# Optimization experiments

Measured on AMD Instinct MI355X. Metric: run time of the kernel, lower is better.

## Reference

```python
import jax, jax.numpy as jnp
import numpy as np

B, N_QUBITS, N_LAYERS = 128, 14, 4


def _rx(theta):
    c = jnp.cos(theta / 2).astype(jnp.complex64)
    s = (-1j) * jnp.sin(theta / 2).astype(jnp.complex64)
    return jnp.stack([jnp.stack([c, s], -1), jnp.stack([s, c], -1)], -2)


def _ry(theta):
    c = jnp.cos(theta / 2)
    s = jnp.sin(theta / 2)
    return jnp.stack([jnp.stack([c, -s], -1), jnp.stack([s, c], -1)], -2).astype(jnp.complex64)


def _rz(theta):
    p = jnp.exp((-0.5j) * theta.astype(jnp.complex64))
    q = jnp.exp((0.5j) * theta.astype(jnp.complex64))
    z = jnp.zeros_like(p)
    return jnp.stack([jnp.stack([p, z], -1), jnp.stack([z, q], -1)], -2)


def _apply_1q(state, U, wire):
    # state: (B, 2, 2, ..., 2); U: (2,2) shared or (B,2,2) per-sample
    s = jnp.moveaxis(state, wire + 1, 1)
    if U.ndim == 2:
        s = jnp.einsum('ij,bj...->bi...', U, s)
    else:
        s = jnp.einsum('bij,bj...->bi...', U, s)
    return jnp.moveaxis(s, 1, wire + 1)


def _cnot(state, c, t):
    s = jnp.moveaxis(state, (c + 1, t + 1), (1, 2))  # (B, 2c, 2t, rest)
    s = jnp.concatenate([s[:, :1], s[:, 1:, ::-1]], axis=1)  # flip target where control=1
    return jnp.moveaxis(s, (1, 2), (c + 1, t + 1))


def _layer(state, rx_l, ry_l, rz_l, ent_l, n):
    for i in range(n):
        state = _apply_1q(state, _rx(rx_l[i]), i)
        state = _apply_1q(state, _ry(ry_l[i]), i)
        state = _apply_1q(state, _rz(rz_l[i]), i)
    for i in range(n - 1):
        state = _cnot(state, i, i + 1)
        state = _apply_1q(state, _rz(ent_l[i]), i + 1)
    return state


def _circuit(x, rx_p, ry_p, rz_p, ent_p):
    b, n = x.shape
    n_layers = rx_p.shape[0]
    scaled = jnp.tanh(x) * np.pi  # angle encoding, matches torch.tanh(x)*pi
    state = jnp.zeros((b,) + (2,) * n, jnp.complex64)
    state = state.at[(slice(None),) + (0,) * n].set(1.0)  # |0...0> per sample
    for i in range(n):  # per-sample RY encoding
        state = _apply_1q(state, _ry(scaled[:, i]), i)
    for l in range(n_layers):
        state = _layer(state, rx_p[l], ry_p[l], rz_p[l], ent_p[l], n)
    probs = state.real ** 2 + state.imag ** 2  # (B, 2, ..., 2) real
    outs = []
    for i in range(n):  # <Z_i> = P(bit_i=0) - P(bit_i=1)
        p = jnp.moveaxis(probs, i + 1, 1).reshape(b, 2, -1).sum(-1)
        outs.append(p[:, 0] - p[:, 1])
    return jnp.stack(outs, -1)  # (B, n_qubits)


def setup_inputs() -> dict:
    key = jax.random.key(0)
    k1, k2, k3, k4, k5 = jax.random.split(key, 5)
    return {
        'x': jax.random.normal(k1, (B, N_QUBITS), jnp.float32),
        'params_rx': jax.random.normal(k2, (N_LAYERS, N_QUBITS), jnp.float32),
        'params_ry': jax.random.normal(k3, (N_LAYERS, N_QUBITS), jnp.float32),
        'params_rz': jax.random.normal(k4, (N_LAYERS, N_QUBITS), jnp.float32),
        'params_entangle': jax.random.normal(k5, (N_LAYERS, N_QUBITS - 1), jnp.float32),
    }


def reference(x, params_rx, params_ry, params_rz, params_entangle):
    return _circuit(x, params_rx, params_ry, params_rz, params_entangle)
```

## Files before the change

kernel.cpp:

```cpp
#include <hip/hip_runtime.h>
#include <math.h>

#define NQ 14
#define NL 4
#define NS (1 << NQ)
#define NT 1024
#define APT (NS / NT)

struct c32 { float x, y; };
__device__ __forceinline__ c32 cmul(c32 a, c32 b) { return {a.x*b.x - a.y*b.y, a.x*b.y + a.y*b.x}; }
__device__ __forceinline__ c32 cadd(c32 a, c32 b) { return {a.x + b.x, a.y + b.y}; }

template<int L> __device__ __forceinline__ int permP(int y) {
    if constexpr (L == 0) return y;
    else if constexpr (L == 1) return y ^ (y >> 1);
    else if constexpr (L == 2) return y ^ (y >> 2);
    else if constexpr (L == 3) { int t = y ^ (y >> 1); return t ^ (t >> 2); }
    else return y ^ (y >> 4);
}

__device__ __forceinline__ void gate8(c32* v, const float* U, const int s) {
    c32 u00={U[0],U[1]}, u01={U[2],U[3]}, u10={U[4],U[5]}, u11={U[6],U[7]};
    #pragma unroll
    for (int k = 0; k < 8; ++k) {
        if (k & s) continue;
        c32 A = v[k], B = v[k | s];
        v[k]     = cadd(cmul(u00, A), cmul(u01, B));
        v[k | s] = cadd(cmul(u10, A), cmul(u11, B));
    }
}

__device__ __forceinline__ void gate8sw(c32* v, const float* U, const int s, const int sw) {
    c32 u00 = sw ? c32{U[6],U[7]} : c32{U[0],U[1]};
    c32 u01 = sw ? c32{U[4],U[5]} : c32{U[2],U[3]};
    c32 u10 = sw ? c32{U[2],U[3]} : c32{U[4],U[5]};
    c32 u11 = sw ? c32{U[0],U[1]} : c32{U[6],U[7]};
    #pragma unroll
    for (int k = 0; k < 8; ++k) {
        if (k & s) continue;
        c32 A = v[k], B = v[k | s];
        v[k]     = cadd(cmul(u00, A), cmul(u01, B));
        v[k | s] = cadd(cmul(u10, A), cmul(u11, B));
    }
}

template<int L, int PB, bool FUSE>
__device__ __forceinline__ void sweep3(float2* st,
                                       const float* U2, const float* U1, const float* U0,
                                       const float* phlo, const float* phhi, int tid) {
    #pragma unroll 1
    for (int m = 0; m < 2; ++m) {
        const int t  = tid + m*NT;
        const int ib = ((t >> PB) << (PB+3)) | (t & ((1 << PB) - 1));
        c32 v[8]; int ad[8];
        #pragma unroll
        for (int k = 0; k < 8; ++k) {
            int y = ib + (k << PB);
            int a = permP<L>(y);
            ad[k] = a;
            float2 f = st[a];
            c32 vv = {f.x, f.y};
            if constexpr (FUSE) {
                float ang = phlo[y & 127] + phhi[(y >> 7) & 63];
                float sn, cs;
                __sincosf(ang, &sn, &cs);
                vv = { cs*vv.x - sn*vv.y, cs*vv.y + sn*vv.x };
            }
            v[k] = vv;
        }
        gate8(v, U2, 4);
        gate8(v, U1, 2);
        gate8(v, U0, 1);
        #pragma unroll
        for (int k = 0; k < 8; ++k) st[ad[k]] = make_float2(v[k].x, v[k].y);
    }
}

template<int L>
__device__ __forceinline__ void sweep2_43(float2* st, const float* U4, const float* U3, int tid) {
    #pragma unroll 1
    for (int m = 0; m < 4; ++m) {
        const int t  = tid + m*NT;
        const int ib = ((t >> 3) << 5) | (t & 7);
        c32 v[4]; int ad[4];
        #pragma unroll
        for (int k = 0; k < 4; ++k) {
            int y = ib + ((k & 1) << 3) + ((k >> 1) << 4);
            int a = permP<L>(y);
            ad[k] = a;
            float2 f = st[a];
            v[k] = {f.x, f.y};
        }
        {
            c32 u00={U4[0],U4[1]}, u01={U4[2],U4[3]}, u10={U4[4],U4[5]}, u11={U4[6],U4[7]};
            #pragma unroll
            for (int k = 0; k < 4; ++k) {
                if (k & 2) continue;
                c32 A = v[k], B = v[k|2];
                v[k]   = cadd(cmul(u00,A), cmul(u01,B));
                v[k|2] = cadd(cmul(u10,A), cmul(u11,B));
            }
        }
        {
            c32 u00={U3[0],U3[1]}, u01={U3[2],U3[3]}, u10={U3[4],U3[5]}, u11={U3[6],U3[7]};
            #pragma unroll
            for (int k = 0; k < 4; ++k) {
                if (k & 1) continue;
                c32 A = v[k], B = v[k|1];
                v[k]   = cadd(cmul(u00,A), cmul(u01,B));
                v[k|1] = cadd(cmul(u10,A), cmul(u11,B));
            }
        }
        #pragma unroll
        for (int k = 0; k < 4; ++k) st[ad[k]] = make_float2(v[k].x, v[k].y);
    }
}

template<int L>
__device__ __forceinline__ void sweep_own(float2* st,
                                          const float* U11, const float* U12, const float* U13,
                                          int tid) {
    const int t4   = tid & 15;
    const int base = tid << 4;
    #pragma unroll 1
    for (int m = 0; m < 2; ++m) {
        c32 v[8]; int ad[8];
        #pragma unroll
        for (int s = 0; s < 8; ++s) {
            int e = ((m << 3) | s) ^ t4;
            int a = permP<L>(base | e);
            ad[s] = a;
            float2 f = st[a];
            v[s] = {f.x, f.y};
        }
        gate8sw(v, U11, 4, (t4 >> 2) & 1);
        gate8sw(v, U12, 2, (t4 >> 1) & 1);
        gate8sw(v, U13, 1,  t4       & 1);
        #pragma unroll
        for (int s = 0; s < 8; ++s) st[ad[s]] = make_float2(v[s].x, v[s].y);
    }
}

template<int L>
__device__ __forceinline__ void do_layer(float2* st, float (*UmL)[8],
                                         const float* phlo, const float* phhi, int tid) {
    constexpr bool F = (L > 0);
    sweep3<L, 11, F>(st, UmL[0], UmL[1], UmL[2], phlo, phhi, tid);
    __syncthreads();
    sweep3<L, 8, false>(st, UmL[3], UmL[4], UmL[5], nullptr, nullptr, tid);
    __syncthreads();
    sweep3<L, 5, false>(st, UmL[6], UmL[7], UmL[8], nullptr, nullptr, tid);
    __syncthreads();
    sweep2_43<L>(st, UmL[9], UmL[10], tid);
    __syncthreads();
    sweep_own<L>(st, UmL[11], UmL[12], UmL[13], tid);
    __syncthreads();
}

__global__ __launch_bounds__(NT) __attribute__((amdgpu_waves_per_eu(4, 4)))
void qc_kernel(const float* __restrict__ x,
               const float* __restrict__ prx,
               const float* __restrict__ pry,
               const float* __restrict__ prz,
               const float* __restrict__ pent,
               float* __restrict__ out)
{
    __shared__ float2 st[NS];
    __shared__ float  Um[NL][NQ][8];
    __shared__ float  tlo[NL][128];
    __shared__ float  thi[NL][64];
    __shared__ float  encc[NQ], encs[NQ];
    __shared__ float  red[NT/64][NQ];

    const int tid = threadIdx.x;
    const int b   = blockIdx.x;

    if (tid < NL*NQ) {
        int l = tid / NQ, q = tid % NQ;
        float hx = 0.5f*prx[l*NQ+q], hy = 0.5f*pry[l*NQ+q], hz = 0.5f*prz[l*NQ+q];
        float cx = cosf(hx), sx = sinf(hx);
        float cy = cosf(hy), sy = sinf(hy);
        float cz = cosf(hz), sz = sinf(hz);
        c32 m00 = { cy*cx,  sy*sx };
        c32 m01 = {-sy*cx, -cy*sx };
        c32 m10 = { sy*cx, -cy*sx };
        c32 m11 = { cy*cx, -sy*sx };
        c32 e0 = {cz, -sz}, e1 = {cz, sz};
        c32 u00 = cmul(e0, m00), u01 = cmul(e0, m01);
        c32 u10 = cmul(e1, m10), u11 = cmul(e1, m11);
        float* U = Um[l][q];
        U[0]=u00.x; U[1]=u00.y; U[2]=u01.x; U[3]=u01.y;
        U[4]=u10.x; U[5]=u10.y; U[6]=u11.x; U[7]=u11.y;
    } else if (tid >= 64 && tid < 64 + NL*192) {
        int t2 = tid - 64;
        int l = t2 / 192, r = t2 % 192;
        if (r < 128) {
            float a = 0.f;
            for (int p = 0; p < 7; ++p) {
                float th = 0.5f * pent[l*(NQ-1) + (12 - p)];
                a += ((r >> p) & 1) ? th : -th;
            }
            tlo[l][r] = a;
        } else {
            int m = r - 128;
            float a = 0.f;
            for (int p = 0; p < 6; ++p) {
                float th = 0.5f * pent[l*(NQ-1) + (5 - p)];
                a += ((m >> p) & 1) ? th : -th;
            }
            thi[l][m] = a;
        }
    } else if (tid >= 960 && tid < 960 + NQ) {
        int i = tid - 960;
        float th = tanhf(x[b*NQ + i]) * 3.14159265358979323846f;
        encc[i] = cosf(0.5f*th);
        encs[i] = sinf(0.5f*th);
    }
    __syncthreads();

    {
        float prodLow = 1.f;
        #pragma unroll
        for (int p = 0; p < 10; ++p) {
            prodLow *= ((tid >> p) & 1) ? encs[13-p] : encc[13-p];
        }
        #pragma unroll
        for (int j = 0; j < APT; ++j) {
            float a = prodLow;
            a *= (j & 1) ? encs[3] : encc[3];
            a *= (j & 2) ? encs[2] : encc[2];
            a *= (j & 4) ? encs[1] : encc[1];
            a *= (j & 8) ? encs[0] : encc[0];
            st[tid + j*NT] = make_float2(a, 0.f);
        }
    }
    __syncthreads();

    do_layer<0>(st, Um[0], nullptr, nullptr, tid);
    do_layer<1>(st, Um[1], tlo[0], thi[0], tid);
    do_layer<2>(st, Um[2], tlo[1], thi[1], tid);
    do_layer<3>(st, Um[3], tlo[2], thi[2], tid);

    float acc[NQ];
    #pragma unroll
    for (int i = 0; i < NQ; ++i) acc[i] = 0.f;
    #pragma unroll
    for (int j = 0; j < APT; ++j) {
        int y = tid + j*NT;
        int a = permP<4>(y);
        float2 v = st[a];
        float ang = tlo[NL-1][y & 127] + thi[NL-1][(y >> 7) & 63];
        float sn, cs;
        __sincosf(ang, &sn, &cs);
        float re = cs*v.x - sn*v.y;
        float im = cs*v.y + sn*v.x;
        float pr = re*re + im*im;
        #pragma unroll
        for (int p = 0; p < NQ; ++p) {
            acc[NQ-1-p] += ((y >> p) & 1) ? -pr : pr;
        }
    }
    #pragma unroll
    for (int off = 32; off >= 1; off >>= 1) {
        #pragma unroll
        for (int i = 0; i < NQ; ++i)
            acc[i] += __shfl_down(acc[i], off, 64);
    }
    const int wid = tid >> 6, lane = tid & 63;
    if (lane == 0) {
        #pragma unroll
        for (int i = 0; i < NQ; ++i) red[wid][i] = acc[i];
    }
    __syncthreads();
    if (tid < NQ) {
        float s = 0.f;
        #pragma unroll
        for (int w = 0; w < NT/64; ++w) s += red[w][tid];
        out[b*NQ + tid] = s;
    }
}

extern "C" void kernel_launch(void* const* d_in, const int* in_sizes, int n_in,
                              void* d_out, int out_size, void* d_ws, size_t ws_size,
                              hipStream_t stream) {
    (void)d_ws; (void)ws_size; (void)n_in; (void)out_size;
    const float* x    = (const float*)d_in[0];
    const float* prx  = (const float*)d_in[1];
    const float* pry  = (const float*)d_in[2];
    const float* prz  = (const float*)d_in[3];
    const float* pent = (const float*)d_in[4];
    float* out = (float*)d_out;
    const int B = in_sizes[0] / NQ;
    qc_kernel<<<B, NT, 0, stream>>>(x, prx, pry, prz, pent, out);
}
```

Before: 143.8 us.

## Split each sample's statevector across two cooperating blocks with global-memory exchange

Adds a kernel that spreads each sample's 2^14-amplitude state over two workgroups of 8192 amplitudes each, doubling the block count to 256 so more compute units stay busy. Each layer's qubit-0 gate is applied by exchanging the partner half through a global workspace, coordinated by release/acquire flags and spin-waits, and the final expectation values are combined through a partial-sum buffer. The first layer is built directly from the product-state encoding, so it skips separate sweeps. This adds global traffic, a memset launch and spin-waits that rely on both partner blocks being resident at once, which carries a deadlock risk if they are not. It falls back to the old kernel when the workspace is too small.

```diff
diff --git a/kernel.cpp b/kernel.cpp
--- a/kernel.cpp
+++ b/kernel.cpp
@@ -7,17 +7,12 @@
 #define NT 1024
 #define APT (NS / NT)
 
+#define NTS 1024
+#define NSH 8192
+
 struct c32 { float x, y; };
 __device__ __forceinline__ c32 cmul(c32 a, c32 b) { return {a.x*b.x - a.y*b.y, a.x*b.y + a.y*b.x}; }
 __device__ __forceinline__ c32 cadd(c32 a, c32 b) { return {a.x + b.x, a.y + b.y}; }
-
-template<int L> __device__ __forceinline__ int permP(int y) {
-    if constexpr (L == 0) return y;
-    else if constexpr (L == 1) return y ^ (y >> 1);
-    else if constexpr (L == 2) return y ^ (y >> 2);
-    else if constexpr (L == 3) { int t = y ^ (y >> 1); return t ^ (t >> 2); }
-    else return y ^ (y >> 4);
-}
 
 __device__ __forceinline__ void gate8(c32* v, const float* U, const int s) {
     c32 u00={U[0],U[1]}, u01={U[2],U[3]}, u10={U[4],U[5]}, u11={U[6],U[7]};
@@ -44,137 +39,10 @@
     }
 }
 
-template<int L, int PB, bool FUSE>
-__device__ __forceinline__ void sweep3(float2* st,
-                                       const float* U2, const float* U1, const float* U0,
-                                       const float* phlo, const float* phhi, int tid) {
-    #pragma unroll 1
-    for (int m = 0; m < 2; ++m) {
-        const int t  = tid + m*NT;
-        const int ib = ((t >> PB) << (PB+3)) | (t & ((1 << PB) - 1));
-        c32 v[8]; int ad[8];
-        #pragma unroll
-        for (int k = 0; k < 8; ++k) {
-            int y = ib + (k << PB);
-            int a = permP<L>(y);
-            ad[k] = a;
-            float2 f = st[a];
-            c32 vv = {f.x, f.y};
-            if constexpr (FUSE) {
-                float ang = phlo[y & 127] + phhi[(y >> 7) & 63];
-                float sn, cs;
-                __sincosf(ang, &sn, &cs);
-                vv = { cs*vv.x - sn*vv.y, cs*vv.y + sn*vv.x };
-            }
-            v[k] = vv;
-        }
-        gate8(v, U2, 4);
-        gate8(v, U1, 2);
-        gate8(v, U0, 1);
-        #pragma unroll
-        for (int k = 0; k < 8; ++k) st[ad[k]] = make_float2(v[k].x, v[k].y);
-    }
-}
-
-template<int L>
-__device__ __forceinline__ void sweep2_43(float2* st, const float* U4, const float* U3, int tid) {
-    #pragma unroll 1
-    for (int m = 0; m < 4; ++m) {
-        const int t  = tid + m*NT;
-        const int ib = ((t >> 3) << 5) | (t & 7);
-        c32 v[4]; int ad[4];
-        #pragma unroll
-        for (int k = 0; k < 4; ++k) {
-            int y = ib + ((k & 1) << 3) + ((k >> 1) << 4);
-            int a = permP<L>(y);
-            ad[k] = a;
-            float2 f = st[a];
-            v[k] = {f.x, f.y};
-        }
-        {
-            c32 u00={U4[0],U4[1]}, u01={U4[2],U4[3]}, u10={U4[4],U4[5]}, u11={U4[6],U4[7]};
-            #pragma unroll
-            for (int k = 0; k < 4; ++k) {
-                if (k & 2) continue;
-                c32 A = v[k], B = v[k|2];
-                v[k]   = cadd(cmul(u00,A), cmul(u01,B));
-                v[k|2] = cadd(cmul(u10,A), cmul(u11,B));
-            }
-        }
-        {
-            c32 u00={U3[0],U3[1]}, u01={U3[2],U3[3]}, u10={U3[4],U3[5]}, u11={U3[6],U3[7]};
-            #pragma unroll
-            for (int k = 0; k < 4; ++k) {
-                if (k & 1) continue;
-                c32 A = v[k], B = v[k|1];
-                v[k]   = cadd(cmul(u00,A), cmul(u01,B));
-                v[k|1] = cadd(cmul(u10,A), cmul(u11,B));
-            }
-        }
-        #pragma unroll
-        for (int k = 0; k < 4; ++k) st[ad[k]] = make_float2(v[k].x, v[k].y);
-    }
-}
-
-template<int L>
-__device__ __forceinline__ void sweep_own(float2* st,
-                                          const float* U11, const float* U12, const float* U13,
-                                          int tid) {
-    const int t4   = tid & 15;
-    const int base = tid << 4;
-    #pragma unroll 1
-    for (int m = 0; m < 2; ++m) {
-        c32 v[8]; int ad[8];
-        #pragma unroll
-        for (int s = 0; s < 8; ++s) {
-            int e = ((m << 3) | s) ^ t4;
-            int a = permP<L>(base | e);
-            ad[s] = a;
-            float2 f = st[a];
-            v[s] = {f.x, f.y};
-        }
-        gate8sw(v, U11, 4, (t4 >> 2) & 1);
-        gate8sw(v, U12, 2, (t4 >> 1) & 1);
-        gate8sw(v, U13, 1,  t4       & 1);
-        #pragma unroll
-        for (int s = 0; s < 8; ++s) st[ad[s]] = make_float2(v[s].x, v[s].y);
-    }
-}
-
-template<int L>
-__device__ __forceinline__ void do_layer(float2* st, float (*UmL)[8],
-                                         const float* phlo, const float* phhi, int tid) {
-    constexpr bool F = (L > 0);
-    sweep3<L, 11, F>(st, UmL[0], UmL[1], UmL[2], phlo, phhi, tid);
-    __syncthreads();
-    sweep3<L, 8, false>(st, UmL[3], UmL[4], UmL[5], nullptr, nullptr, tid);
-    __syncthreads();
-    sweep3<L, 5, false>(st, UmL[6], UmL[7], UmL[8], nullptr, nullptr, tid);
-    __syncthreads();
-    sweep2_43<L>(st, UmL[9], UmL[10], tid);
-    __syncthreads();
-    sweep_own<L>(st, UmL[11], UmL[12], UmL[13], tid);
-    __syncthreads();
-}
-
-__global__ __launch_bounds__(NT) __attribute__((amdgpu_waves_per_eu(4, 4)))
-void qc_kernel(const float* __restrict__ x,
-               const float* __restrict__ prx,
-               const float* __restrict__ pry,
-               const float* __restrict__ prz,
-               const float* __restrict__ pent,
-               float* __restrict__ out)
-{
-    __shared__ float2 st[NS];
-    __shared__ float  Um[NL][NQ][8];
-    __shared__ float  tlo[NL][128];
-    __shared__ float  thi[NL][64];
-    __shared__ float  encc[NQ], encs[NQ];
-    __shared__ float  red[NT/64][NQ];
-
-    const int tid = threadIdx.x;
-    const int b   = blockIdx.x;
-
+__device__ __forceinline__ void precompute(const float* x, const float* prx, const float* pry,
+                                           const float* prz, const float* pent,
+                                           float (*Um)[NQ][8], float (*tlo)[128], float (*thi)[64],
+                                           float* encc, float* encs, int tid, int samp) {
     if (tid < NL*NQ) {
         int l = tid / NQ, q = tid % NQ;
         float hx = 0.5f*prx[l*NQ+q], hy = 0.5f*pry[l*NQ+q], hz = 0.5f*prz[l*NQ+q];
@@ -212,18 +80,373 @@
         }
     } else if (tid >= 960 && tid < 960 + NQ) {
         int i = tid - 960;
-        float th = tanhf(x[b*NQ + i]) * 3.14159265358979323846f;
+        float th = tanhf(x[samp*NQ + i]) * 3.14159265358979323846f;
         encc[i] = cosf(0.5f*th);
         encs[i] = sinf(0.5f*th);
     }
+}
+
+
+__device__ __forceinline__ void flag_set(int* p, int v) {
+    __threadfence();
+    __hip_atomic_store(p, v, __ATOMIC_RELEASE, __HIP_MEMORY_SCOPE_AGENT);
+}
+__device__ __forceinline__ void flag_wait(int* p, int v) {
+    while (__hip_atomic_load(p, __ATOMIC_ACQUIRE, __HIP_MEMORY_SCOPE_AGENT) != v)
+        __builtin_amdgcn_s_sleep(2);
+    __threadfence();
+}
+
+template<int PB>
+__device__ __forceinline__ void sweepS3(float2* st, const float* U2, const float* U1,
+                                        const float* U0s, int tid) {
+    const int ib = ((tid >> PB) << (PB+3)) | (tid & ((1 << PB) - 1));
+    c32 v[8];
+    #pragma unroll
+    for (int k = 0; k < 8; ++k) { float2 f = st[ib + (k << PB)]; v[k] = {f.x, f.y}; }
+    gate8(v, U2, 4); gate8(v, U1, 2); gate8(v, U0s, 1);
+    #pragma unroll
+    for (int k = 0; k < 8; ++k) st[ib + (k << PB)] = make_float2(v[k].x, v[k].y);
+}
+
+__device__ __forceinline__ void sweepS1(float2* st, const float* U, int tid) {
+    c32 u00={U[0],U[1]}, u01={U[2],U[3]}, u10={U[4],U[5]}, u11={U[6],U[7]};
+    #pragma unroll
+    for (int m = 0; m < 4; ++m) {
+        int u = tid + m*NTS;
+        int i = ((u >> 3) << 4) | (u & 7);
+        float2 f0 = st[i], f1 = st[i | 8];
+        c32 A = {f0.x, f0.y}, B = {f1.x, f1.y};
+        c32 r0 = cadd(cmul(u00, A), cmul(u01, B));
+        c32 r1 = cadd(cmul(u10, A), cmul(u11, B));
+        st[i]     = make_float2(r0.x, r0.y);
+        st[i | 8] = make_float2(r1.x, r1.y);
+    }
+}
+
+__device__ __forceinline__ void sweepSA(float2* st, const float2* pd, const float* Uq0,
+                                        const float* U11, const float* U12, const float* U13,
+                                        int tid, int h) {
+    const int t7 = tid & 7;
+    const int base = tid << 3;
+    c32 cm = h ? c32{Uq0[6], Uq0[7]} : c32{Uq0[0], Uq0[1]};
+    c32 cp = h ? c32{Uq0[4], Uq0[5]} : c32{Uq0[2], Uq0[3]};
+    c32 p[8];
+    #pragma unroll
+    for (int s = 0; s < 8; ++s) { float2 g = pd[base | (s ^ t7)]; p[s] = {g.x, g.y}; }
+    c32 v[8];
+    #pragma unroll
+    for (int s = 0; s < 8; ++s) {
+        float2 f = st[base | (s ^ t7)];
+        v[s] = cadd(cmul(cm, c32{f.x, f.y}), cmul(cp, p[s]));
+    }
+    gate8sw(v, U11, 4, (t7 >> 2) & 1);
+    gate8sw(v, U12, 2, (t7 >> 1) & 1);
+    gate8sw(v, U13, 1,  t7       & 1);
+    #pragma unroll
+    for (int s = 0; s < 8; ++s) st[base | (s ^ t7)] = make_float2(v[s].x, v[s].y);
+}
+
+__device__ __forceinline__ void gatherS(float2* st, float2* myd, const float* phlo,
+                                        const float* phhi, int tid, int hb12) {
+    c32 tmp[8];
+    #pragma unroll
+    for (int m = 0; m < 8; ++m) {
+        int z = tid + m*NTS;
+        int a = (z ^ (z >> 1)) ^ hb12;
+        float2 f = st[a];
+        float ang = phlo[z & 127] + phhi[(z >> 7) & 63];
+        float sn, cs;
+        __sincosf(ang, &sn, &cs);
+        tmp[m] = { cs*f.x - sn*f.y, cs*f.y + sn*f.x };
+    }
+    __syncthreads();
+    #pragma unroll
+    for (int m = 0; m < 8; ++m) {
+        int z = tid + m*NTS;
+        float2 val = make_float2(tmp[m].x, tmp[m].y);
+        st[z]  = val;
+        myd[z] = val;
+    }
+}
+
+__global__ __launch_bounds__(NTS)
+void qc_split(const float* __restrict__ x,
+              const float* __restrict__ prx,
+              const float* __restrict__ pry,
+              const float* __restrict__ prz,
+              const float* __restrict__ pent,
+              float* __restrict__ out,
+              float2* __restrict__ pdata,
+              int* __restrict__ dumpF,
+              int* __restrict__ consF,
+              float* __restrict__ part)
+{
+    __shared__ float2 st[NSH];
+    __shared__ float  Um[NL][NQ][8];
+    __shared__ float  tlo[NL][128];
+    __shared__ float  thi[NL][64];
+    __shared__ float  encc[NQ], encs[NQ];
+    __shared__ float  red[NTS/64][NQ];
+
+    const int tid  = threadIdx.x;
+    const int bid  = blockIdx.x;
+    const int samp = bid >> 1;
+    const int h    = bid & 1;
+    const int pb   = bid ^ 1;
+    const int hb12 = h << 12;
+    float2* myd      = pdata + (size_t)bid * NSH;
+    const float2* pd = pdata + (size_t)pb  * NSH;
+
+    precompute(x, prx, pry, prz, pent, Um, tlo, thi, encc, encs, tid, samp);
+    __syncthreads();
+
+    {
+        const int t7 = tid & 7;
+        const int base = tid << 3;
+        const float* U0 = Um[0][0];
+        float c0 = encc[0], s0 = encs[0];
+        c32 vh = h ? c32{U0[4]*c0 + U0[6]*s0, U0[5]*c0 + U0[7]*s0}
+                   : c32{U0[0]*c0 + U0[2]*s0, U0[1]*c0 + U0[3]*s0};
+        float ph = 1.f;
+        #pragma unroll
+        for (int p = 3; p <= 12; ++p)
+            ph *= ((tid >> (p-3)) & 1) ? encs[13-p] : encc[13-p];
+        c32 v[8];
+        #pragma unroll
+        for (int s = 0; s < 8; ++s) {
+            int e = s ^ t7;
+            float f = ph * ((e & 4) ? encs[11] : encc[11])
+                         * ((e & 2) ? encs[12] : encc[12])
+                         * ((e & 1) ? encs[13] : encc[13]);
+            v[s] = { vh.x * f, vh.y * f };
+        }
+        gate8sw(v, Um[0][11], 4, (t7 >> 2) & 1);
+        gate8sw(v, Um[0][12], 2, (t7 >> 1) & 1);
+        gate8sw(v, Um[0][13], 1,  t7       & 1);
+        #pragma unroll
+        for (int s = 0; s < 8; ++s) st[base | (s ^ t7)] = make_float2(v[s].x, v[s].y);
+    }
+    __syncthreads();
+
+    sweepS3<10>(st, Um[0][1], Um[0][2], Um[0][3], tid); __syncthreads();
+    sweepS3<7 >(st, Um[0][4], Um[0][5], Um[0][6], tid); __syncthreads();
+    sweepS3<4 >(st, Um[0][7], Um[0][8], Um[0][9], tid); __syncthreads();
+    sweepS1(st, Um[0][10], tid); __syncthreads();
+    gatherS(st, myd, tlo[0], thi[0], tid, hb12);
+    __syncthreads();
+    if (tid == 0) flag_set(&dumpF[bid], 1);
+
+    #pragma unroll 1
+    for (int l = 1; l < NL; ++l) {
+        if (tid == 0) flag_wait(&dumpF[pb], l);
+        __syncthreads();
+        sweepSA(st, pd, Um[l][0], Um[l][11], Um[l][12], Um[l][13], tid, h);
+        __syncthreads();
+        if (l < 3 && tid == 0) flag_set(&consF[bid], l);
+        sweepS3<10>(st, Um[l][1], Um[l][2], Um[l][3], tid); __syncthreads();
+        sweepS3<7 >(st, Um[l][4], Um[l][5], Um[l][6], tid); __syncthreads();
+        sweepS3<4 >(st, Um[l][7], Um[l][8], Um[l][9], tid); __syncthreads();
+        sweepS1(st, Um[l][10], tid); __syncthreads();
+        if (l < 3) {
+            if (tid == 0) flag_wait(&consF[pb], l);
+            __syncthreads();
+            gatherS(st, myd, tlo[l], thi[l], tid, hb12);
+            __syncthreads();
+            if (tid == 0) flag_set(&dumpF[bid], l + 1);
+        }
+    }
+
+    float acc[NQ];
+    #pragma unroll
+    for (int i = 0; i < NQ; ++i) acc[i] = 0.f;
+    #pragma unroll
+    for (int m = 0; m < 8; ++m) {
+        int z = tid + m*NTS;
+        int a = (z ^ (z >> 1)) ^ hb12;
+        float2 f = st[a];
+        float ang = tlo[NL-1][z & 127] + thi[NL-1][(z >> 7) & 63];
+        float sn, cs;
+        __sincosf(ang, &sn, &cs);
+        float re = cs*f.x - sn*f.y;
+        float im = cs*f.y + sn*f.x;
+        float pr = re*re + im*im;
+        acc[0] += h ? -pr : pr;
+        #pragma unroll
+        for (int p = 0; p <= 12; ++p)
+            acc[13-p] += ((z >> p) & 1) ? -pr : pr;
+    }
+    #pragma unroll
+    for (int off = 32; off >= 1; off >>= 1) {
+        #pragma unroll
+        for (int i = 0; i < NQ; ++i)
+            acc[i] += __shfl_down(acc[i], off, 64);
+    }
+    const int wid = tid >> 6, lane = tid & 63;
+    if (lane == 0) {
+        #pragma unroll
+        for (int i = 0; i < NQ; ++i) red[wid][i] = acc[i];
+    }
+    __syncthreads();
+    float s = 0.f;
+    if (tid < NQ) {
+        #pragma unroll
+        for (int w = 0; w < NTS/64; ++w) s += red[w][tid];
+    }
+    if (h == 1) {
+        if (tid < NQ) part[bid*16 + tid] = s;
+        __syncthreads();
+        if (tid == 0) flag_set(&dumpF[bid], 4);
+    } else {
+        if (tid == 0) flag_wait(&dumpF[pb], 4);
+        __syncthreads();
+        if (tid < NQ) out[samp*NQ + tid] = s + part[pb*16 + tid];
+    }
+}
+
+template<int L> __device__ __forceinline__ int permP(int y) {
+    if constexpr (L == 0) return y;
+    else if constexpr (L == 1) return y ^ (y >> 1);
+    else if constexpr (L == 2) return y ^ (y >> 2);
+    else if constexpr (L == 3) { int t = y ^ (y >> 1); return t ^ (t >> 2); }
+    else return y ^ (y >> 4);
+}
+
+template<int L, int PB, bool FUSE>
+__device__ __forceinline__ void sweep3(float2* st, const float* U2, const float* U1,
+                                       const float* U0, const float* phlo, const float* phhi, int tid) {
+    #pragma unroll 1
+    for (int m = 0; m < 2; ++m) {
+        const int t  = tid + m*NT;
+        const int ib = ((t >> PB) << (PB+3)) | (t & ((1 << PB) - 1));
+        c32 v[8]; int ad[8];
+        #pragma unroll
+        for (int k = 0; k < 8; ++k) {
+            int y = ib + (k << PB);
+            int a = permP<L>(y);
+            ad[k] = a;
+            float2 f = st[a];
+            c32 vv = {f.x, f.y};
+            if constexpr (FUSE) {
+                float ang = phlo[y & 127] + phhi[(y >> 7) & 63];
+                float sn, cs;
+                __sincosf(ang, &sn, &cs);
+                vv = { cs*vv.x - sn*vv.y, cs*vv.y + sn*vv.x };
+            }
+            v[k] = vv;
+        }
+        gate8(v, U2, 4); gate8(v, U1, 2); gate8(v, U0, 1);
+        #pragma unroll
+        for (int k = 0; k < 8; ++k) st[ad[k]] = make_float2(v[k].x, v[k].y);
+    }
+}
+
+template<int L>
+__device__ __forceinline__ void sweep2_43(float2* st, const float* U4, const float* U3, int tid) {
+    #pragma unroll 1
+    for (int m = 0; m < 4; ++m) {
+        const int t  = tid + m*NT;
+        const int ib = ((t >> 3) << 5) | (t & 7);
+        c32 v[4]; int ad[4];
+        #pragma unroll
+        for (int k = 0; k < 4; ++k) {
+            int y = ib + ((k & 1) << 3) + ((k >> 1) << 4);
+            int a = permP<L>(y);
+            ad[k] = a;
+            float2 f = st[a];
+            v[k] = {f.x, f.y};
+        }
+        {
+            c32 u00={U4[0],U4[1]}, u01={U4[2],U4[3]}, u10={U4[4],U4[5]}, u11={U4[6],U4[7]};
+            #pragma unroll
+            for (int k = 0; k < 4; ++k) {
+                if (k & 2) continue;
+                c32 A = v[k], B = v[k|2];
+                v[k]   = cadd(cmul(u00,A), cmul(u01,B));
+                v[k|2] = cadd(cmul(u10,A), cmul(u11,B));
+            }
+        }
+        {
+            c32 u00={U3[0],U3[1]}, u01={U3[2],U3[3]}, u10={U3[4],U3[5]}, u11={U3[6],U3[7]};
+            #pragma unroll
+            for (int k = 0; k < 4; ++k) {
+                if (k & 1) continue;
+                c32 A = v[k], B = v[k|1];
+                v[k]   = cadd(cmul(u00,A), cmul(u01,B));
+                v[k|1] = cadd(cmul(u10,A), cmul(u11,B));
+            }
+        }
+        #pragma unroll
+        for (int k = 0; k < 4; ++k) st[ad[k]] = make_float2(v[k].x, v[k].y);
+    }
+}
+
+template<int L>
+__device__ __forceinline__ void sweep_own(float2* st, const float* U11, const float* U12,
+                                          const float* U13, int tid) {
+    const int t4   = tid & 15;
+    const int base = tid << 4;
+    #pragma unroll 1
+    for (int m = 0; m < 2; ++m) {
+        c32 v[8]; int ad[8];
+        #pragma unroll
+        for (int s = 0; s < 8; ++s) {
+            int e = ((m << 3) | s) ^ t4;
+            int a = permP<L>(base | e);
+            ad[s] = a;
+            float2 f = st[a];
+            v[s] = {f.x, f.y};
+        }
+        gate8sw(v, U11, 4, (t4 >> 2) & 1);
+        gate8sw(v, U12, 2, (t4 >> 1) & 1);
+        gate8sw(v, U13, 1,  t4       & 1);
+        #pragma unroll
+        for (int s = 0; s < 8; ++s) st[ad[s]] = make_float2(v[s].x, v[s].y);
+    }
+}
+
+template<int L>
+__device__ __forceinline__ void do_layer(float2* st, float (*UmL)[8],
+                                         const float* phlo, const float* phhi, int tid) {
+    constexpr bool F = (L > 0);
+    sweep3<L, 11, F>(st, UmL[0], UmL[1], UmL[2], phlo, phhi, tid);
+    __syncthreads();
+    sweep3<L, 8, false>(st, UmL[3], UmL[4], UmL[5], nullptr, nullptr, tid);
+    __syncthreads();
+    sweep3<L, 5, false>(st, UmL[6], UmL[7], UmL[8], nullptr, nullptr, tid);
+    __syncthreads();
+    sweep2_43<L>(st, UmL[9], UmL[10], tid);
+    __syncthreads();
+    sweep_own<L>(st, UmL[11], UmL[12], UmL[13], tid);
+    __syncthreads();
+}
+
+__global__ __launch_bounds__(NT) __attribute__((amdgpu_waves_per_eu(4, 4)))
+void qc_kernel(const float* __restrict__ x,
+               const float* __restrict__ prx,
+               const float* __restrict__ pry,
+               const float* __restrict__ prz,
+               const float* __restrict__ pent,
+               float* __restrict__ out)
+{
+    __shared__ float2 st[NS];
+    __shared__ float  Um[NL][NQ][8];
+    __shared__ float  tlo[NL][128];
+    __shared__ float  thi[NL][64];
+    __shared__ float  encc[NQ], encs[NQ];
+    __shared__ float  red[NT/64][NQ];
+
+    const int tid = threadIdx.x;
+    const int b   = blockIdx.x;
+
+    precompute(x, prx, pry, prz, pent, Um, tlo, thi, encc, encs, tid, b);
     __syncthreads();
 
     {
         float prodLow = 1.f;
         #pragma unroll
-        for (int p = 0; p < 10; ++p) {
+        for (int p = 0; p < 10; ++p)
             prodLow *= ((tid >> p) & 1) ? encs[13-p] : encc[13-p];
-        }
         #pragma unroll
         for (int j = 0; j < APT; ++j) {
             float a = prodLow;
@@ -256,9 +479,8 @@
         float im = cs*v.y + sn*v.x;
         float pr = re*re + im*im;
         #pragma unroll
-        for (int p = 0; p < NQ; ++p) {
+        for (int p = 0; p < NQ; ++p)
             acc[NQ-1-p] += ((y >> p) & 1) ? -pr : pr;
-        }
     }
     #pragma unroll
     for (int off = 32; off >= 1; off >>= 1) {
@@ -283,7 +505,7 @@
 extern "C" void kernel_launch(void* const* d_in, const int* in_sizes, int n_in,
                               void* d_out, int out_size, void* d_ws, size_t ws_size,
                               hipStream_t stream) {
-    (void)d_ws; (void)ws_size; (void)n_in; (void)out_size;
+    (void)n_in; (void)out_size;
     const float* x    = (const float*)d_in[0];
     const float* prx  = (const float*)d_in[1];
     const float* pry  = (const float*)d_in[2];
@@ -291,5 +513,24 @@
     const float* pent = (const float*)d_in[4];
     float* out = (float*)d_out;
     const int B = in_sizes[0] / NQ;
-    qc_kernel<<<B, NT, 0, stream>>>(x, prx, pry, prz, pent, out);
-}
+    const int nb = 2 * B;
+
+    const size_t pdataBytes = (size_t)nb * NSH * sizeof(float2);
+    const size_t flagsOff   = pdataBytes;
+    const size_t consOff    = flagsOff + 2048;
+    const size_t partOff    = flagsOff + 4096;
+    const size_t need       = partOff + (size_t)nb * 16 * sizeof(float);
+
+    if (ws_size >= need) {
+        char* wsb = (char*)d_ws;
+        float2* pdata = (float2*)wsb;
+        int*    dumpF = (int*)(wsb + flagsOff);
+        int*    consF = (int*)(wsb + consOff);
+        float*  part  = (float*)(wsb + partOff);
+        hipMemsetAsync(wsb + flagsOff, 0, 4096, stream);
+        qc_split<<<nb, NTS, 0, stream>>>(x, prx, pry, prz, pent, out,
+                                         pdata, dumpF, consF, part);
+    } else {
+        qc_kernel<<<B, NT, 0, stream>>>(x, prx, pry, prz, pent, out);
+    }
+}
```

Measured after the change: 250.7 us. +74.4%, slower.
